# Performance work log

Measured on AMD Instinct MI355X. Metric: run time of the kernel, lower is better.

The kernel has to match this reference:

```python
import jax, jax.numpy as jnp
import numpy as np

T, B = 50, 512
S, A, BEL, H, E, M = 256, 32, 1024, 1024, 1024, 256
MIN_STD = 0.1


def setup_inputs() -> dict:
    key = jax.random.key(0)
    ks = jax.random.split(key, 24)
    def rn(k, shape, scale=1.0):
        return jax.random.normal(k, shape, dtype=jnp.float32) * scale
    w = 0.05  # weight init scale
    return {
        "prev_state": rn(ks[0], (B, S)),
        "actions": rn(ks[1], (T, B, A)),
        "prev_belief": rn(ks[2], (B, BEL)),
        "observations": rn(ks[3], (T, B, E)),
        "nonterminals": jnp.ones((T, B, 1), dtype=jnp.float32),
        "map_embeddings": rn(ks[4], (T, B, M)),
        "map_embeddings_post": rn(ks[5], (T, B, M)),
        "noise_prior": rn(ks[6], (T, B, S)),
        "noise_post": rn(ks[7], (T, B, S)),
        "W_sa": rn(ks[8], (BEL, S + A + M), w), "b_sa": jnp.zeros((BEL,), jnp.float32),
        "W_ih": rn(ks[9], (3 * BEL, BEL), w), "b_ih": jnp.zeros((3 * BEL,), jnp.float32),
        "W_hh": rn(ks[10], (3 * BEL, BEL), w), "b_hh": jnp.zeros((3 * BEL,), jnp.float32),
        "W_bp": rn(ks[11], (H, BEL), w), "b_bp": jnp.zeros((H,), jnp.float32),
        "W_sp": rn(ks[12], (2 * S, H), w), "b_sp": jnp.zeros((2 * S,), jnp.float32),
        "W_bq": rn(ks[13], (H, BEL + E + M), w), "b_bq": jnp.zeros((H,), jnp.float32),
        "W_sq": rn(ks[14], (2 * S, H), w), "b_sq": jnp.zeros((2 * S,), jnp.float32),
    }


def reference(prev_state, actions, prev_belief, observations, nonterminals,
              map_embeddings, map_embeddings_post, noise_prior, noise_post,
              W_sa, b_sa, W_ih, b_ih, W_hh, b_hh,
              W_bp, b_bp, W_sp, b_sp, W_bq, b_bq, W_sq, b_sq):
    relu = jax.nn.relu
    def lin(x, W, b):
        return x @ W.T + b

    def gru(x, h):  # torch.nn.GRUCell math
        gi = x @ W_ih.T + b_ih
        gh = h @ W_hh.T + b_hh
        i_r, i_z, i_n = jnp.split(gi, 3, axis=1)
        h_r, h_z, h_n = jnp.split(gh, 3, axis=1)
        r = jax.nn.sigmoid(i_r + h_r)
        z = jax.nn.sigmoid(i_z + h_z)
        n = jnp.tanh(i_n + r * h_n)
        return (1.0 - z) * n + z * h

    def std(raw):
        return jnp.minimum(jax.nn.softplus(raw) + MIN_STD, 5.0)

    def step(carry, xs):
        belief, post_state = carry
        a, obs, nt, me, mp, np_, nq = xs
        s = post_state * nt
        hid = relu(lin(jnp.concatenate([s, a, me], axis=1), W_sa, b_sa))
        belief = gru(hid, belief)
        # prior p(z_t | h_t)
        hp = relu(lin(belief, W_bp, b_bp))
        p_mean, p_raw = jnp.split(lin(hp, W_sp, b_sp), 2, axis=1)
        p_std = std(p_raw)
        p_state = p_mean + p_std * np_
        # posterior q(z_t | h_t, e_t, m_t)
        hq = relu(lin(jnp.concatenate([belief, obs, mp], axis=1), W_bq, b_bq))
        q_mean, q_raw = jnp.split(lin(hq, W_sq, b_sq), 2, axis=1)
        q_std = std(q_raw)
        q_state = q_mean + q_std * nq
        return (belief, q_state), (belief, p_state, p_mean, p_std, q_state, q_mean, q_std)

    _, outs = jax.lax.scan(
        step, (prev_belief, prev_state),
        (actions, observations, nonterminals, map_embeddings,
         map_embeddings_post, noise_prior, noise_post))
    return outs  # 7 arrays, each (T, B, *)
```

## Files before the change

kernel.cpp:

```cpp
#include <hip/hip_runtime.h>
#include <hip/hip_bf16.h>

#define NT 50
#define NB 512
#define SD 256
#define BD 1024
#define HD 1024
#define ED 1024
#define MD 256
#define NBLK 512
#define GSZ (NBLK * 256)
#define PGSZ (1024 * 256)
#define K1BIG 0x40000000
#define NSLOT 256

typedef __attribute__((ext_vector_type(8))) short bf16x8;
typedef __attribute__((ext_vector_type(4))) float f32x4;

__device__ __forceinline__ void gload_lds16(const void* g, void* l) {
  __builtin_amdgcn_global_load_lds(
      (const __attribute__((address_space(1))) void*)g,
      (__attribute__((address_space(3))) void*)l, 16, 0, 0);
}

__device__ __forceinline__ void cload16_async(const void* a, f32x4* r) {
  asm volatile("global_load_dwordx4 %0, %1, off sc0 sc1" : "=&v"(*r) : "v"(a) : "memory");
}
__device__ __forceinline__ void cload4_async(const void* a, float* r) {
  asm volatile("global_load_dword %0, %1, off sc0 sc1" : "=&v"(*r) : "v"(a) : "memory");
}
#define VMWAIT(N)                                        \
  asm volatile("s_waitcnt vmcnt(" #N ")" ::: "memory");  \
  __builtin_amdgcn_sched_barrier(0);

__device__ __forceinline__ void cstore16(void* g, f32x4 v) {
  asm volatile("global_store_dwordx4 %0, %1, off sc0 sc1" :: "v"(g), "v"(v) : "memory");
}
__device__ __forceinline__ void cstore4(void* g, float v) {
  asm volatile("global_store_dword %0, %1, off sc0 sc1" :: "v"(g), "v"(v) : "memory");
}
__device__ __forceinline__ void cstore2(void* g, unsigned v) {
  asm volatile("global_store_short %0, %1, off sc0 sc1" :: "v"(g), "v"(v) : "memory");
}
__device__ __forceinline__ void ntstore16(void* g, f32x4 v) {
  asm volatile("global_store_dwordx4 %0, %1, off nt" :: "v"(g), "v"(v) : "memory");
}
__device__ __forceinline__ void ntstore4(void* g, float v) {
  asm volatile("global_store_dword %0, %1, off nt" :: "v"(g), "v"(v) : "memory");
}

__device__ __forceinline__ float sigmoidf_(float x) { return 1.0f / (1.0f + __expf(-x)); }
__device__ __forceinline__ float softplusf_(float x) {
  return (x > 0.0f) ? (x + log1pf(__expf(-x))) : log1pf(__expf(x));
}
__device__ __forceinline__ unsigned short bfb(float x) {
  __hip_bfloat16 h = __float2bfloat16(x);
  return __builtin_bit_cast(unsigned short, h);
}

__device__ __forceinline__ void gbar(unsigned* cnt, int slot, int b) {
  asm volatile("s_waitcnt vmcnt(0) lgkmcnt(0)" ::: "memory");
  __syncthreads();
  if (threadIdx.x == 0) {
    unsigned* lc = cnt + slot * 128 + (b & 7) * 16;
    unsigned* gc = cnt + NSLOT * 128 + slot * 16;
    unsigned* fl = cnt + NSLOT * 144 + slot * 16;
    unsigned old = __hip_atomic_fetch_add(lc, 1u, __ATOMIC_RELAXED, __HIP_MEMORY_SCOPE_AGENT);
    if (old == (NBLK / 8 - 1)) {
      unsigned g = __hip_atomic_fetch_add(gc, 1u, __ATOMIC_RELAXED, __HIP_MEMORY_SCOPE_AGENT);
      if (g == 7u)
        __hip_atomic_store(fl, 1u, __ATOMIC_RELAXED, __HIP_MEMORY_SCOPE_AGENT);
    }
    while (__hip_atomic_load(fl, __ATOMIC_RELAXED, __HIP_MEMORY_SCOPE_AGENT) == 0u)
      __builtin_amdgcn_s_sleep(2);
  }
  __syncthreads();
}

__device__ __noinline__ void gemm64(
    int EPI, char* lds,
    const __hip_bfloat16* __restrict__ A1, int lda1,
    const __hip_bfloat16* __restrict__ A2, int lda2, int K1,
    const __hip_bfloat16* __restrict__ Wr, int ldw, int nIter,
    const float* __restrict__ bias, const float* __restrict__ Cadd,
    float* __restrict__ Cf, __hip_bfloat16* __restrict__ Cb, int ldc, int m0) {
  const int tid = threadIdx.x;
  const int lane = tid & 63, w = tid >> 6;
  const int wr = w >> 1, wc = w & 1;
  f32x4 acc[2][2] = {};
  const __hip_bfloat16* a1r = A1 + (size_t)(m0 + lane) * lda1;
  const __hip_bfloat16* a2r = A2 ? (A2 + (size_t)(m0 + lane) * lda2) : a1r;
  const __hip_bfloat16* wrow = Wr + (size_t)lane * ldw;

  f32x4 rA0, rA1;
  auto issueA = [&](int it) {
    const int k0 = it << 6;
    const __hip_bfloat16* as = (k0 < K1) ? (a1r + k0) : (a2r + (k0 - K1));
    cload16_async(as + (2 * w) * 8, &rA0);
    cload16_async(as + (2 * w + 1) * 8, &rA1);
  };
  auto writeA = [&](int it) {
    char* la = lds + ((it & 1) << 14);
    *(f32x4*)(la + (2 * w) * 1024 + lane * 16) = rA0;
    *(f32x4*)(la + (2 * w + 1) * 1024 + lane * 16) = rA1;
  };
  auto stageW = [&](int it) {
    const int k0 = it << 6;
    char* lb = lds + ((it & 1) << 14) + 8192;
    gload_lds16(wrow + k0 + (2 * w) * 8, lb + (2 * w) * 1024);
    gload_lds16(wrow + k0 + (2 * w + 1) * 8, lb + (2 * w + 1) * 1024);
  };

  issueA(0);
  VMWAIT(0)
  writeA(0);
  stageW(0);

  const int kq = lane >> 4, r15 = lane & 15;
  for (int i = 0; i < nIter; ++i) {
    __syncthreads();
    if (i + 1 < nIter) {
      issueA(i + 1);
      stageW(i + 1);
    }
    const char* la = lds + ((i & 1) << 14);
    const char* lb = la + 8192;
#pragma unroll
    for (int s = 0; s < 2; ++s) {
      bf16x8 af[2], bfr[2];
#pragma unroll
      for (int m = 0; m < 2; ++m)
        af[m] = *(const bf16x8*)(la + (size_t)((s * 4 + kq) * 64 + wr * 32 + m * 16 + r15) * 16);
#pragma unroll
      for (int n = 0; n < 2; ++n)
        bfr[n] = *(const bf16x8*)(lb + (size_t)((s * 4 + kq) * 64 + wc * 32 + n * 16 + r15) * 16);
#pragma unroll
      for (int m = 0; m < 2; ++m)
#pragma unroll
        for (int n = 0; n < 2; ++n)
          acc[m][n] = __builtin_amdgcn_mfma_f32_16x16x32_bf16(af[m], bfr[n], acc[m][n], 0, 0, 0);
    }
    if (i + 1 < nIter) {
      VMWAIT(2)
      writeA(i + 1);
    }
  }

  const int rg = lane >> 4;
  float ad[2][2][4];
  if (EPI == 3) {
#pragma unroll
    for (int m = 0; m < 2; ++m)
#pragma unroll
      for (int n = 0; n < 2; ++n) {
        const int col = wc * 32 + n * 16 + r15;
#pragma unroll
        for (int i2 = 0; i2 < 4; ++i2) {
          const int row = m0 + wr * 32 + m * 16 + rg * 4 + i2;
          cload4_async(Cadd + (size_t)row * ldc + col, &ad[m][n][i2]);
        }
      }
    VMWAIT(0)
  }
#pragma unroll
  for (int m = 0; m < 2; ++m) {
#pragma unroll
    for (int n = 0; n < 2; ++n) {
      const int col = wc * 32 + n * 16 + r15;
      const float bv = bias ? bias[col] : 0.0f;
#pragma unroll
      for (int i2 = 0; i2 < 4; ++i2) {
        const int row = m0 + wr * 32 + m * 16 + rg * 4 + i2;
        float v = acc[m][n][i2] + bv;
        if (EPI == 3) v += ad[m][n][i2];
        if (EPI != 0) {
          v = v > 0.0f ? v : 0.0f;
          cstore2(Cb + (size_t)row * ldc + col, (unsigned)bfb(v));
        } else {
          cstore4(Cf + (size_t)row * ldc + col, v);
        }
      }
    }
  }
}

__device__ __noinline__ void gemm_head64(
    char* lds, const __hip_bfloat16* __restrict__ A,
    const __hip_bfloat16* __restrict__ Wr, const float* __restrict__ bias,
    const float* __restrict__ noise, float* __restrict__ st_o, float* __restrict__ mn_o,
    float* __restrict__ sd_o, const float* __restrict__ ntn,
    __hip_bfloat16* __restrict__ sprev, int isq, int n0, int m0) {
  const int tid = threadIdx.x;
  const int lane = tid & 63, w = tid >> 6;
  const int wr = w >> 1, wc = w & 1;
  f32x4 acc[2][2] = {};
  const __hip_bfloat16* ar = A + (size_t)(m0 + lane) * BD;
  const __hip_bfloat16* wrow = Wr + (size_t)lane * BD;

  f32x4 rA0, rA1;
  auto issueA = [&](int it) {
    const int k0 = it << 6;
    cload16_async(ar + k0 + (2 * w) * 8, &rA0);
    cload16_async(ar + k0 + (2 * w + 1) * 8, &rA1);
  };
  auto writeA = [&](int it) {
    char* la = lds + ((it & 1) << 14);
    *(f32x4*)(la + (2 * w) * 1024 + lane * 16) = rA0;
    *(f32x4*)(la + (2 * w + 1) * 1024 + lane * 16) = rA1;
  };
  auto stageW = [&](int it) {
    const int k0 = it << 6;
    char* lb = lds + ((it & 1) << 14) + 8192;
    gload_lds16(wrow + k0 + (2 * w) * 8, lb + (2 * w) * 1024);
    gload_lds16(wrow + k0 + (2 * w + 1) * 8, lb + (2 * w + 1) * 1024);
  };

  issueA(0);
  VMWAIT(0)
  writeA(0);
  stageW(0);

  const int kq = lane >> 4, r15 = lane & 15;
  for (int i = 0; i < 16; ++i) {
    __syncthreads();
    if (i + 1 < 16) {
      issueA(i + 1);
      stageW(i + 1);
    }
    const char* la = lds + ((i & 1) << 14);
    const char* lb = la + 8192;
#pragma unroll
    for (int s = 0; s < 2; ++s) {
      bf16x8 af[2], bfr[2];
#pragma unroll
      for (int m = 0; m < 2; ++m)
        af[m] = *(const bf16x8*)(la + (size_t)((s * 4 + kq) * 64 + wr * 32 + m * 16 + r15) * 16);
#pragma unroll
      for (int n = 0; n < 2; ++n)
        bfr[n] = *(const bf16x8*)(lb + (size_t)((s * 4 + kq) * 64 + wc * 32 + n * 16 + r15) * 16);
#pragma unroll
      for (int m = 0; m < 2; ++m)
#pragma unroll
        for (int n = 0; n < 2; ++n)
          acc[m][n] = __builtin_amdgcn_mfma_f32_16x16x32_bf16(af[m], bfr[n], acc[m][n], 0, 0, 0);
    }
    if (i + 1 < 16) {
      VMWAIT(2)
      writeA(i + 1);
    }
  }

  const int rg = lane >> 4;
  const bool even = (r15 & 1) == 0;
#pragma unroll
  for (int m = 0; m < 2; ++m) {
#pragma unroll
    for (int n = 0; n < 2; ++n) {
      const int col = n0 + wc * 32 + n * 16 + r15;
      const int j = col >> 1;
      const float bv = bias[col];
#pragma unroll
      for (int i2 = 0; i2 < 4; ++i2) {
        const int row = m0 + wr * 32 + m * 16 + rg * 4 + i2;
        float v = acc[m][n][i2] + bv;
        float partner = __shfl_xor(v, 1);
        float mean = even ? v : partner;
        float raw = even ? partner : v;
        float sd = fminf(softplusf_(raw) + 0.1f, 5.0f);
        const size_t o = (size_t)row * SD + j;
        if (even) {
          float st = mean + sd * noise[o];
          ntstore4(mn_o + o, mean);
          ntstore4(st_o + o, st);
          if (isq) cstore2(sprev + o, (unsigned)bfb(st * ntn[row]));
        } else {
          ntstore4(sd_o + o, sd);
        }
      }
    }
  }
}

struct Args {
  const float *prev_state, *actions, *prev_belief, *observations, *nonterminals,
      *me, *mp, *noise_p, *noise_q,
      *W_sa, *b_sa, *W_ih, *b_ih, *W_hh, *b_hh,
      *W_bp, *b_bp, *W_sp, *b_sp, *W_bq, *b_bq, *W_sq, *b_sq;
  float* out;
  unsigned* cnt;
  __hip_bfloat16 *Wsa, *Wih, *Whh, *Wbp, *Wbq, *Wsp, *Wsq;
  __hip_bfloat16 *actme, *obsmp, *sprev, *bel, *hid, *hpb, *hqb;
  float *gi, *gh, *hq_obs;
  float *bsp_ro, *bsq_ro;
};

__global__ __launch_bounds__(256) void prep(Args P) {
  const int gtid = blockIdx.x * 256 + threadIdx.x;
  for (int i = gtid; i < BD * 576; i += PGSZ) {
    int r = i / 576, k = i - r * 576;
    P.Wsa[i] = __float2bfloat16(k < 544 ? P.W_sa[(size_t)r * 544 + k] : 0.0f);
  }
  for (int i = gtid; i < 3 * BD * BD; i += PGSZ) P.Wih[i] = __float2bfloat16(P.W_ih[i]);
  for (int i = gtid; i < 3 * BD * BD; i += PGSZ) P.Whh[i] = __float2bfloat16(P.W_hh[i]);
  for (int i = gtid; i < HD * BD; i += PGSZ) P.Wbp[i] = __float2bfloat16(P.W_bp[i]);
  for (int i = gtid; i < HD * 2304; i += PGSZ) P.Wbq[i] = __float2bfloat16(P.W_bq[i]);
  for (int i = gtid; i < 512 * HD; i += PGSZ) {
    int r = i >> 10, k = i & 1023;
    int dr = (r < 256) ? (2 * r) : (2 * (r - 256) + 1);
    P.Wsp[(size_t)dr * 1024 + k] = __float2bfloat16(P.W_sp[i]);
    P.Wsq[(size_t)dr * 1024 + k] = __float2bfloat16(P.W_sq[i]);
  }
  for (int i = gtid; i < 512; i += PGSZ) {
    int dr = (i < 256) ? (2 * i) : (2 * (i - 256) + 1);
    P.bsp_ro[dr] = P.b_sp[i];
    P.bsq_ro[dr] = P.b_sq[i];
  }
  for (int i = gtid; i < NT * NB * 320; i += PGSZ) {
    int tb = i / 320, j = i - tb * 320;
    float v = (j < 32) ? P.actions[(size_t)tb * 32 + j]
                       : (j < 288 ? P.me[(size_t)tb * 256 + (j - 32)] : 0.0f);
    P.actme[i] = __float2bfloat16(v);
  }
  for (int i = gtid; i < NB * 1280; i += PGSZ) {
    int bb = i / 1280, j = i - bb * 1280;
    float v = (j < ED) ? P.observations[(size_t)bb * ED + j] : P.mp[(size_t)bb * MD + (j - ED)];
    P.obsmp[i] = __float2bfloat16(v);
  }
  for (int i = gtid; i < NB * SD; i += PGSZ) {
    int r = i >> 8;
    P.sprev[i] = __float2bfloat16(P.prev_state[i] * P.nonterminals[r]);
  }
  for (int i = gtid; i < NB * BD; i += PGSZ) P.bel[i] = __float2bfloat16(P.prev_belief[i]);
}

__global__ __launch_bounds__(256, 4) void mega(Args P) {
  __shared__ alignas(16) char lds[32768];
  const int b = blockIdx.x, tid = threadIdx.x;
  const int gtid = b * 256 + tid;

  const size_t o_ps = (size_t)NT * NB * BD;
  const size_t blk = (size_t)NT * NB * SD;

  for (int t = 0; t < NT; ++t) {
    const int s0 = t * 5;
    if (b < 128) {
      const int u = (b & 7) * 16 + (b >> 3), n = u >> 3, m = u & 7;
      gemm64(1, lds, P.sprev, SD, P.actme + (size_t)t * NB * 320, 320, 256,
             P.Wsa + (size_t)n * 64 * 576, 576, 9,
             P.b_sa + n * 64, nullptr, nullptr, P.hid + n * 64, BD, m * 64);
    } else {
      const int b2 = b - 128;
      const int u = (b2 & 7) * 48 + (b2 >> 3), n = u >> 3, m = u & 7;
      gemm64(0, lds, P.bel, BD, nullptr, 0, K1BIG,
             P.Whh + (size_t)n * 64 * BD, BD, 16,
             P.b_hh + n * 64, nullptr, P.gh + n * 64, nullptr, 3 * BD, m * 64);
    }
    gbar(P.cnt, s0 + 0, b);
    if (b < 384) {
      const int u = (b & 7) * 48 + (b >> 3), n = u >> 3, m = u & 7;
      gemm64(0, lds, P.hid, BD, nullptr, 0, K1BIG,
             P.Wih + (size_t)n * 64 * BD, BD, 16,
             P.b_ih + n * 64, nullptr, P.gi + n * 64, nullptr, 3 * BD, m * 64);
    } else if (t == 0) {
      const int b2 = b - 384;
      const int u = (b2 & 7) * 16 + (b2 >> 3), n = u >> 3, m = u & 7;
      gemm64(0, lds, P.obsmp, 1280, nullptr, 0, K1BIG,
             P.Wbq + (size_t)n * 64 * 2304 + 1024, 2304, 20,
             nullptr, nullptr, P.hq_obs + n * 64, nullptr, 1024, m * 64);
    }
    gbar(P.cnt, s0 + 1, b);
    if (gtid < 65536) {
      const int bb = gtid >> 7, j0 = (gtid & 127) << 3;
      const float* gib = P.gi + (size_t)bb * 3072 + j0;
      const float* ghb = P.gh + (size_t)bb * 3072 + j0;
      f32x4 ir0, ir1, iz0, iz1, in0, in1, hr0, hr1, hz0, hz1, hn0, hn1, hbv;
      cload16_async(gib, &ir0);
      cload16_async(gib + 4, &ir1);
      cload16_async(gib + 1024, &iz0);
      cload16_async(gib + 1028, &iz1);
      cload16_async(gib + 2048, &in0);
      cload16_async(gib + 2052, &in1);
      cload16_async(ghb, &hr0);
      cload16_async(ghb + 4, &hr1);
      cload16_async(ghb + 1024, &hz0);
      cload16_async(ghb + 1028, &hz1);
      cload16_async(ghb + 2048, &hn0);
      cload16_async(ghb + 2052, &hn1);
      cload16_async(P.bel + (size_t)bb * BD + j0, &hbv);
      VMWAIT(0)
      bf16x8 hb = __builtin_bit_cast(bf16x8, hbv);
      float o[8];
      unsigned short nb[8];
#pragma unroll
      for (int k = 0; k < 8; ++k) {
        float gr = (k < 4 ? ir0[k] : ir1[k - 4]) + (k < 4 ? hr0[k] : hr1[k - 4]);
        float gz = (k < 4 ? iz0[k] : iz1[k - 4]) + (k < 4 ? hz0[k] : hz1[k - 4]);
        float hn = (k < 4 ? hn0[k] : hn1[k - 4]);
        float in_ = (k < 4 ? in0[k] : in1[k - 4]);
        float r_ = sigmoidf_(gr);
        float z_ = sigmoidf_(gz);
        float n_ = tanhf(in_ + r_ * hn);
        __hip_bfloat16 hv16 = __builtin_bit_cast(__hip_bfloat16, (unsigned short)hb[k]);
        float hv = __bfloat162float(hv16);
        float bel = (1.0f - z_) * n_ + z_ * hv;
        o[k] = bel;
        nb[k] = bfb(bel);
      }
      float* ob = P.out + (size_t)t * NB * BD + (size_t)bb * BD + j0;
      ntstore16(ob, f32x4{o[0], o[1], o[2], o[3]});
      ntstore16(ob + 4, f32x4{o[4], o[5], o[6], o[7]});
      cstore16(P.bel + (size_t)bb * BD + j0, __builtin_bit_cast(f32x4, *(bf16x8*)nb));
    } else if (gtid < 65536 + 40960 && t + 1 < NT) {
      const int k = gtid - 65536;
      const int bb = k / 80, rr = k - bb * 80, j0 = rr << 4;
      const float* src = (j0 < ED)
          ? (P.observations + (size_t)(t + 1) * NB * ED + (size_t)bb * ED + j0)
          : (P.mp + (size_t)(t + 1) * NB * MD + (size_t)bb * MD + (j0 - ED));
      unsigned short nb[16];
#pragma unroll
      for (int q = 0; q < 4; ++q) {
        f32x4 v = *(const f32x4*)(src + q * 4);
#pragma unroll
        for (int kk = 0; kk < 4; ++kk) nb[q * 4 + kk] = bfb(v[kk]);
      }
      cstore16(P.obsmp + (size_t)bb * 1280 + j0, __builtin_bit_cast(f32x4, *(bf16x8*)nb));
      cstore16(P.obsmp + (size_t)bb * 1280 + j0 + 8, __builtin_bit_cast(f32x4, *(bf16x8*)(nb + 8)));
    }
    gbar(P.cnt, s0 + 2, b);
    if (b < 128) {
      const int u = (b & 7) * 16 + (b >> 3), n = u >> 3, m = u & 7;
      gemm64(1, lds, P.bel, BD, nullptr, 0, K1BIG,
             P.Wbp + (size_t)n * 64 * BD, BD, 16,
             P.b_bp + n * 64, nullptr, nullptr, P.hpb + n * 64, HD, m * 64);
    } else if (b < 256) {
      const int b2 = b - 128;
      const int u = (b2 & 7) * 16 + (b2 >> 3), n = u >> 3, m = u & 7;
      gemm64(3, lds, P.bel, BD, nullptr, 0, K1BIG,
             P.Wbq + (size_t)n * 64 * 2304, 2304, 16,
             P.b_bq + n * 64, P.hq_obs + n * 64, nullptr, P.hqb + n * 64, HD, m * 64);
    }
    gbar(P.cnt, s0 + 3, b);
    if (b < 128) {
      const int u = (b & 7) * 16 + (b >> 3);
      const int pq = u >> 6, rr = u & 63, n = rr >> 3, m = rr & 7;
      const float* ntn = P.nonterminals + (size_t)((t + 1 < NT) ? t + 1 : t) * NB;
      const size_t to = (size_t)t * NB * SD;
      if (pq == 0)
        gemm_head64(lds, P.hpb, P.Wsp + (size_t)n * 64 * BD, P.bsp_ro,
                    P.noise_p + to, P.out + o_ps + to, P.out + o_ps + blk + to,
                    P.out + o_ps + 2 * blk + to, ntn, P.sprev, 0, n * 64, m * 64);
      else
        gemm_head64(lds, P.hqb, P.Wsq + (size_t)n * 64 * BD, P.bsq_ro,
                    P.noise_q + to, P.out + o_ps + 3 * blk + to, P.out + o_ps + 4 * blk + to,
                    P.out + o_ps + 5 * blk + to, ntn, P.sprev, 1, n * 64, m * 64);
    } else if (b < 256 && t + 1 < NT) {
      const int b2 = b - 128;
      const int u = (b2 & 7) * 16 + (b2 >> 3), n = u >> 3, m = u & 7;
      gemm64(0, lds, P.obsmp, 1280, nullptr, 0, K1BIG,
             P.Wbq + (size_t)n * 64 * 2304 + 1024, 2304, 20,
             nullptr, nullptr, P.hq_obs + n * 64, nullptr, 1024, m * 64);
    }
    gbar(P.cnt, s0 + 4, b);
  }
}


extern "C" void kernel_launch(void* const* d_in, const int* in_sizes, int n_in,
                              void* d_out, int out_size, void* d_ws, size_t ws_size,
                              hipStream_t stream) {
  Args P;
  P.prev_state = (const float*)d_in[0];
  P.actions = (const float*)d_in[1];
  P.prev_belief = (const float*)d_in[2];
  P.observations = (const float*)d_in[3];
  P.nonterminals = (const float*)d_in[4];
  P.me = (const float*)d_in[5];
  P.mp = (const float*)d_in[6];
  P.noise_p = (const float*)d_in[7];
  P.noise_q = (const float*)d_in[8];
  P.W_sa = (const float*)d_in[9];  P.b_sa = (const float*)d_in[10];
  P.W_ih = (const float*)d_in[11]; P.b_ih = (const float*)d_in[12];
  P.W_hh = (const float*)d_in[13]; P.b_hh = (const float*)d_in[14];
  P.W_bp = (const float*)d_in[15]; P.b_bp = (const float*)d_in[16];
  P.W_sp = (const float*)d_in[17]; P.b_sp = (const float*)d_in[18];
  P.W_bq = (const float*)d_in[19]; P.b_bq = (const float*)d_in[20];
  P.W_sq = (const float*)d_in[21]; P.b_sq = (const float*)d_in[22];
  P.out = (float*)d_out;

  char* p = (char*)d_ws;
  auto carve = [&](size_t bytes) -> char* {
    char* r = p;
    p += (bytes + 255) & ~(size_t)255;
    return r;
  };
  const size_t cnt_bytes = (size_t)NSLOT * 160 * 4;
  P.cnt = (unsigned*)carve(cnt_bytes);
  P.Wsa = (__hip_bfloat16*)carve((size_t)BD * 576 * 2);
  P.Wih = (__hip_bfloat16*)carve((size_t)3 * BD * BD * 2);
  P.Whh = (__hip_bfloat16*)carve((size_t)3 * BD * BD * 2);
  P.Wbp = (__hip_bfloat16*)carve((size_t)HD * BD * 2);
  P.Wbq = (__hip_bfloat16*)carve((size_t)HD * 2304 * 2);
  P.Wsp = (__hip_bfloat16*)carve((size_t)512 * HD * 2);
  P.Wsq = (__hip_bfloat16*)carve((size_t)512 * HD * 2);
  P.bsp_ro = (float*)carve(512 * 4);
  P.bsq_ro = (float*)carve(512 * 4);
  P.actme = (__hip_bfloat16*)carve((size_t)NT * NB * 320 * 2);
  P.obsmp = (__hip_bfloat16*)carve((size_t)NB * 1280 * 2);
  P.sprev = (__hip_bfloat16*)carve((size_t)NB * SD * 2);
  P.bel = (__hip_bfloat16*)carve((size_t)NB * BD * 2);
  P.hid = (__hip_bfloat16*)carve((size_t)NB * BD * 2);
  P.hpb = (__hip_bfloat16*)carve((size_t)NB * HD * 2);
  P.hqb = (__hip_bfloat16*)carve((size_t)NB * HD * 2);
  P.gi = (float*)carve((size_t)NB * 3 * BD * 4);
  P.gh = (float*)carve((size_t)NB * 3 * BD * 4);
  P.hq_obs = (float*)carve((size_t)NB * HD * 4);

  hipMemsetAsync(P.cnt, 0, cnt_bytes, stream);
  prep<<<1024, 256, 0, stream>>>(P);
  mega<<<NBLK, 256, 0, stream>>>(P);
}
```

Measured before the change: 5.713 ms.

## Partition batch rows per XCD and replace grid barriers with per-XCD barriers

Each block reads its hardware XCC id and claims a slot within that XCD. Each XCD then owns 64 batch rows, so each timestep's stages only need a barrier among the blocks of one XCD instead of the whole grid. Because the data a block exchanges now stays inside one XCD's L2, coherent loads and stores drop the sc1 bit and use sc0 only. This relies on the row split matching the XCD mapping and on the startup counting being correct. Each XCD now reads all the weights itself, which adds weight traffic in exchange for lighter synchronisation.

```diff
diff --git a/kernel.cpp b/kernel.cpp
--- a/kernel.cpp
+++ b/kernel.cpp
@@ -9,10 +9,8 @@
 #define ED 1024
 #define MD 256
 #define NBLK 512
-#define GSZ (NBLK * 256)
 #define PGSZ (1024 * 256)
 #define K1BIG 0x40000000
-#define NSLOT 256
 
 typedef __attribute__((ext_vector_type(8))) short bf16x8;
 typedef __attribute__((ext_vector_type(4))) float f32x4;
@@ -23,24 +21,24 @@
       (__attribute__((address_space(3))) void*)l, 16, 0, 0);
 }
 
-__device__ __forceinline__ void cload16_async(const void* a, f32x4* r) {
-  asm volatile("global_load_dwordx4 %0, %1, off sc0 sc1" : "=&v"(*r) : "v"(a) : "memory");
-}
-__device__ __forceinline__ void cload4_async(const void* a, float* r) {
-  asm volatile("global_load_dword %0, %1, off sc0 sc1" : "=&v"(*r) : "v"(a) : "memory");
+__device__ __forceinline__ void aload16(const void* a, f32x4* r) {
+  asm volatile("global_load_dwordx4 %0, %1, off sc0" : "=&v"(*r) : "v"(a) : "memory");
+}
+__device__ __forceinline__ void aload4(const void* a, float* r) {
+  asm volatile("global_load_dword %0, %1, off sc0" : "=&v"(*r) : "v"(a) : "memory");
 }
 #define VMWAIT(N)                                        \
   asm volatile("s_waitcnt vmcnt(" #N ")" ::: "memory");  \
   __builtin_amdgcn_sched_barrier(0);
 
-__device__ __forceinline__ void cstore16(void* g, f32x4 v) {
-  asm volatile("global_store_dwordx4 %0, %1, off sc0 sc1" :: "v"(g), "v"(v) : "memory");
-}
-__device__ __forceinline__ void cstore4(void* g, float v) {
-  asm volatile("global_store_dword %0, %1, off sc0 sc1" :: "v"(g), "v"(v) : "memory");
-}
-__device__ __forceinline__ void cstore2(void* g, unsigned v) {
-  asm volatile("global_store_short %0, %1, off sc0 sc1" :: "v"(g), "v"(v) : "memory");
+__device__ __forceinline__ void astore16(void* g, f32x4 v) {
+  asm volatile("global_store_dwordx4 %0, %1, off sc0" :: "v"(g), "v"(v) : "memory");
+}
+__device__ __forceinline__ void astore4(void* g, float v) {
+  asm volatile("global_store_dword %0, %1, off sc0" :: "v"(g), "v"(v) : "memory");
+}
+__device__ __forceinline__ void astore2(void* g, unsigned v) {
+  asm volatile("global_store_short %0, %1, off sc0" :: "v"(g), "v"(v) : "memory");
 }
 __device__ __forceinline__ void ntstore16(void* g, f32x4 v) {
   asm volatile("global_store_dwordx4 %0, %1, off nt" :: "v"(g), "v"(v) : "memory");
@@ -58,21 +56,14 @@
   return __builtin_bit_cast(unsigned short, h);
 }
 
-__device__ __forceinline__ void gbar(unsigned* cnt, int slot, int b) {
+__device__ __forceinline__ void xbar(unsigned* cnt, int inst, int xcd, int nx) {
   asm volatile("s_waitcnt vmcnt(0) lgkmcnt(0)" ::: "memory");
   __syncthreads();
   if (threadIdx.x == 0) {
-    unsigned* lc = cnt + slot * 128 + (b & 7) * 16;
-    unsigned* gc = cnt + NSLOT * 128 + slot * 16;
-    unsigned* fl = cnt + NSLOT * 144 + slot * 16;
-    unsigned old = __hip_atomic_fetch_add(lc, 1u, __ATOMIC_RELAXED, __HIP_MEMORY_SCOPE_AGENT);
-    if (old == (NBLK / 8 - 1)) {
-      unsigned g = __hip_atomic_fetch_add(gc, 1u, __ATOMIC_RELAXED, __HIP_MEMORY_SCOPE_AGENT);
-      if (g == 7u)
-        __hip_atomic_store(fl, 1u, __ATOMIC_RELAXED, __HIP_MEMORY_SCOPE_AGENT);
-    }
-    while (__hip_atomic_load(fl, __ATOMIC_RELAXED, __HIP_MEMORY_SCOPE_AGENT) == 0u)
-      __builtin_amdgcn_s_sleep(2);
+    unsigned* c = cnt + 256 + (size_t)(inst * 8 + xcd) * 16;
+    __hip_atomic_fetch_add(c, 1u, __ATOMIC_RELAXED, __HIP_MEMORY_SCOPE_AGENT);
+    while (__hip_atomic_load(c, __ATOMIC_RELAXED, __HIP_MEMORY_SCOPE_AGENT) < (unsigned)nx)
+      __builtin_amdgcn_s_sleep(4);
   }
   __syncthreads();
 }
@@ -96,8 +87,8 @@
   auto issueA = [&](int it) {
     const int k0 = it << 6;
     const __hip_bfloat16* as = (k0 < K1) ? (a1r + k0) : (a2r + (k0 - K1));
-    cload16_async(as + (2 * w) * 8, &rA0);
-    cload16_async(as + (2 * w + 1) * 8, &rA1);
+    aload16(as + (2 * w) * 8, &rA0);
+    aload16(as + (2 * w + 1) * 8, &rA1);
   };
   auto writeA = [&](int it) {
     char* la = lds + ((it & 1) << 14);
@@ -111,6 +102,7 @@
     gload_lds16(wrow + k0 + (2 * w + 1) * 8, lb + (2 * w + 1) * 1024);
   };
 
+  __syncthreads();
   issueA(0);
   VMWAIT(0)
   writeA(0);
@@ -157,7 +149,7 @@
 #pragma unroll
         for (int i2 = 0; i2 < 4; ++i2) {
           const int row = m0 + wr * 32 + m * 16 + rg * 4 + i2;
-          cload4_async(Cadd + (size_t)row * ldc + col, &ad[m][n][i2]);
+          aload4(Cadd + (size_t)row * ldc + col, &ad[m][n][i2]);
         }
       }
     VMWAIT(0)
@@ -175,9 +167,9 @@
         if (EPI == 3) v += ad[m][n][i2];
         if (EPI != 0) {
           v = v > 0.0f ? v : 0.0f;
-          cstore2(Cb + (size_t)row * ldc + col, (unsigned)bfb(v));
+          astore2(Cb + (size_t)row * ldc + col, (unsigned)bfb(v));
         } else {
-          cstore4(Cf + (size_t)row * ldc + col, v);
+          astore4(Cf + (size_t)row * ldc + col, v);
         }
       }
     }
@@ -200,8 +192,8 @@
   f32x4 rA0, rA1;
   auto issueA = [&](int it) {
     const int k0 = it << 6;
-    cload16_async(ar + k0 + (2 * w) * 8, &rA0);
-    cload16_async(ar + k0 + (2 * w + 1) * 8, &rA1);
+    aload16(ar + k0 + (2 * w) * 8, &rA0);
+    aload16(ar + k0 + (2 * w + 1) * 8, &rA1);
   };
   auto writeA = [&](int it) {
     char* la = lds + ((it & 1) << 14);
@@ -215,6 +207,7 @@
     gload_lds16(wrow + k0 + (2 * w + 1) * 8, lb + (2 * w + 1) * 1024);
   };
 
+  __syncthreads();
   issueA(0);
   VMWAIT(0)
   writeA(0);
@@ -272,7 +265,7 @@
           float st = mean + sd * noise[o];
           ntstore4(mn_o + o, mean);
           ntstore4(st_o + o, st);
-          if (isq) cstore2(sprev + o, (unsigned)bfb(st * ntn[row]));
+          if (isq) astore2(sprev + o, (unsigned)bfb(st * ntn[row]));
         } else {
           ntstore4(sd_o + o, sd);
         }
@@ -335,58 +328,83 @@
 
 __global__ __launch_bounds__(256, 4) void mega(Args P) {
   __shared__ alignas(16) char lds[32768];
-  const int b = blockIdx.x, tid = threadIdx.x;
-  const int gtid = b * 256 + tid;
-
+  __shared__ int sh[3];
+  const int tid = threadIdx.x;
+
+  if (tid == 0) {
+    unsigned x;
+    asm volatile("s_getreg_b32 %0, hwreg(HW_REG_XCC_ID)" : "=s"(x));
+    x &= 7u;
+    unsigned s = __hip_atomic_fetch_add(P.cnt + x * 16, 1u, __ATOMIC_RELAXED,
+                                        __HIP_MEMORY_SCOPE_AGENT);
+    sh[0] = (int)x;
+    sh[1] = (int)s;
+  }
+  __syncthreads();
+  const int xcd = sh[0], slot = sh[1];
+
+  if (tid == 0) {
+    __hip_atomic_fetch_add(P.cnt + 128, 1u, __ATOMIC_RELAXED, __HIP_MEMORY_SCOPE_AGENT);
+    while (__hip_atomic_load(P.cnt + 128, __ATOMIC_RELAXED, __HIP_MEMORY_SCOPE_AGENT) <
+           (unsigned)NBLK)
+      __builtin_amdgcn_s_sleep(4);
+    sh[2] = (int)__hip_atomic_load(P.cnt + xcd * 16, __ATOMIC_RELAXED,
+                                   __HIP_MEMORY_SCOPE_AGENT);
+  }
+  __syncthreads();
+  const int nx = sh[2];
+  const int m0 = xcd * 64;
   const size_t o_ps = (size_t)NT * NB * BD;
   const size_t blk = (size_t)NT * NB * SD;
 
   for (int t = 0; t < NT; ++t) {
-    const int s0 = t * 5;
-    if (b < 128) {
-      const int u = (b & 7) * 16 + (b >> 3), n = u >> 3, m = u & 7;
-      gemm64(1, lds, P.sprev, SD, P.actme + (size_t)t * NB * 320, 320, 256,
-             P.Wsa + (size_t)n * 64 * 576, 576, 9,
-             P.b_sa + n * 64, nullptr, nullptr, P.hid + n * 64, BD, m * 64);
-    } else {
-      const int b2 = b - 128;
-      const int u = (b2 & 7) * 48 + (b2 >> 3), n = u >> 3, m = u & 7;
-      gemm64(0, lds, P.bel, BD, nullptr, 0, K1BIG,
-             P.Whh + (size_t)n * 64 * BD, BD, 16,
-             P.b_hh + n * 64, nullptr, P.gh + n * 64, nullptr, 3 * BD, m * 64);
-    }
-    gbar(P.cnt, s0 + 0, b);
-    if (b < 384) {
-      const int u = (b & 7) * 48 + (b >> 3), n = u >> 3, m = u & 7;
-      gemm64(0, lds, P.hid, BD, nullptr, 0, K1BIG,
-             P.Wih + (size_t)n * 64 * BD, BD, 16,
-             P.b_ih + n * 64, nullptr, P.gi + n * 64, nullptr, 3 * BD, m * 64);
-    } else if (t == 0) {
-      const int b2 = b - 384;
-      const int u = (b2 & 7) * 16 + (b2 >> 3), n = u >> 3, m = u & 7;
-      gemm64(0, lds, P.obsmp, 1280, nullptr, 0, K1BIG,
-             P.Wbq + (size_t)n * 64 * 2304 + 1024, 2304, 20,
-             nullptr, nullptr, P.hq_obs + n * 64, nullptr, 1024, m * 64);
-    }
-    gbar(P.cnt, s0 + 1, b);
-    if (gtid < 65536) {
-      const int bb = gtid >> 7, j0 = (gtid & 127) << 3;
-      const float* gib = P.gi + (size_t)bb * 3072 + j0;
-      const float* ghb = P.gh + (size_t)bb * 3072 + j0;
+    const int inst = t * 5;
+    for (int tt = slot; tt < 64; tt += nx) {
+      if (tt < 16) {
+        const int n = tt;
+        gemm64(1, lds, P.sprev, SD, P.actme + (size_t)t * NB * 320, 320, 256,
+               P.Wsa + (size_t)n * 64 * 576, 576, 9,
+               P.b_sa + n * 64, nullptr, nullptr, P.hid + n * 64, BD, m0);
+      } else {
+        const int n = tt - 16;
+        gemm64(0, lds, P.bel, BD, nullptr, 0, K1BIG,
+               P.Whh + (size_t)n * 64 * BD, BD, 16,
+               P.b_hh + n * 64, nullptr, P.gh + n * 64, nullptr, 3 * BD, m0);
+      }
+    }
+    xbar(P.cnt, inst + 0, xcd, nx);
+    for (int tt = slot; tt < 64; tt += nx) {
+      if (tt < 48) {
+        const int n = tt;
+        gemm64(0, lds, P.hid, BD, nullptr, 0, K1BIG,
+               P.Wih + (size_t)n * 64 * BD, BD, 16,
+               P.b_ih + n * 64, nullptr, P.gi + n * 64, nullptr, 3 * BD, m0);
+      } else {
+        const int n = tt - 48;
+        gemm64(0, lds, P.obsmp, 1280, nullptr, 0, K1BIG,
+               P.Wbq + (size_t)n * 64 * 2304 + 1024, 2304, 20,
+               nullptr, nullptr, P.hq_obs + n * 64, nullptr, 1024, m0);
+      }
+    }
+    xbar(P.cnt, inst + 1, xcd, nx);
+    for (int u = slot * 256 + tid; u < 8192; u += nx * 256) {
+      const int r = m0 + (u >> 7), j0 = (u & 127) << 3;
+      const float* gib = P.gi + (size_t)r * 3072 + j0;
+      const float* ghb = P.gh + (size_t)r * 3072 + j0;
       f32x4 ir0, ir1, iz0, iz1, in0, in1, hr0, hr1, hz0, hz1, hn0, hn1, hbv;
-      cload16_async(gib, &ir0);
-      cload16_async(gib + 4, &ir1);
-      cload16_async(gib + 1024, &iz0);
-      cload16_async(gib + 1028, &iz1);
-      cload16_async(gib + 2048, &in0);
-      cload16_async(gib + 2052, &in1);
-      cload16_async(ghb, &hr0);
-      cload16_async(ghb + 4, &hr1);
-      cload16_async(ghb + 1024, &hz0);
-      cload16_async(ghb + 1028, &hz1);
-      cload16_async(ghb + 2048, &hn0);
-      cload16_async(ghb + 2052, &hn1);
-      cload16_async(P.bel + (size_t)bb * BD + j0, &hbv);
+      aload16(gib, &ir0);
+      aload16(gib + 4, &ir1);
+      aload16(gib + 1024, &iz0);
+      aload16(gib + 1028, &iz1);
+      aload16(gib + 2048, &in0);
+      aload16(gib + 2052, &in1);
+      aload16(ghb, &hr0);
+      aload16(ghb + 4, &hr1);
+      aload16(ghb + 1024, &hz0);
+      aload16(ghb + 1028, &hz1);
+      aload16(ghb + 2048, &hn0);
+      aload16(ghb + 2052, &hn1);
+      aload16(P.bel + (size_t)r * BD + j0, &hbv);
       VMWAIT(0)
       bf16x8 hb = __builtin_bit_cast(bf16x8, hbv);
       float o[8];
@@ -406,61 +424,60 @@
         o[k] = bel;
         nb[k] = bfb(bel);
       }
-      float* ob = P.out + (size_t)t * NB * BD + (size_t)bb * BD + j0;
+      float* ob = P.out + (size_t)t * NB * BD + (size_t)r * BD + j0;
       ntstore16(ob, f32x4{o[0], o[1], o[2], o[3]});
       ntstore16(ob + 4, f32x4{o[4], o[5], o[6], o[7]});
-      cstore16(P.bel + (size_t)bb * BD + j0, __builtin_bit_cast(f32x4, *(bf16x8*)nb));
-    } else if (gtid < 65536 + 40960 && t + 1 < NT) {
-      const int k = gtid - 65536;
-      const int bb = k / 80, rr = k - bb * 80, j0 = rr << 4;
-      const float* src = (j0 < ED)
-          ? (P.observations + (size_t)(t + 1) * NB * ED + (size_t)bb * ED + j0)
-          : (P.mp + (size_t)(t + 1) * NB * MD + (size_t)bb * MD + (j0 - ED));
-      unsigned short nb[16];
-#pragma unroll
-      for (int q = 0; q < 4; ++q) {
-        f32x4 v = *(const f32x4*)(src + q * 4);
-#pragma unroll
-        for (int kk = 0; kk < 4; ++kk) nb[q * 4 + kk] = bfb(v[kk]);
-      }
-      cstore16(P.obsmp + (size_t)bb * 1280 + j0, __builtin_bit_cast(f32x4, *(bf16x8*)nb));
-      cstore16(P.obsmp + (size_t)bb * 1280 + j0 + 8, __builtin_bit_cast(f32x4, *(bf16x8*)(nb + 8)));
-    }
-    gbar(P.cnt, s0 + 2, b);
-    if (b < 128) {
-      const int u = (b & 7) * 16 + (b >> 3), n = u >> 3, m = u & 7;
-      gemm64(1, lds, P.bel, BD, nullptr, 0, K1BIG,
-             P.Wbp + (size_t)n * 64 * BD, BD, 16,
-             P.b_bp + n * 64, nullptr, nullptr, P.hpb + n * 64, HD, m * 64);
-    } else if (b < 256) {
-      const int b2 = b - 128;
-      const int u = (b2 & 7) * 16 + (b2 >> 3), n = u >> 3, m = u & 7;
-      gemm64(3, lds, P.bel, BD, nullptr, 0, K1BIG,
-             P.Wbq + (size_t)n * 64 * 2304, 2304, 16,
-             P.b_bq + n * 64, P.hq_obs + n * 64, nullptr, P.hqb + n * 64, HD, m * 64);
-    }
-    gbar(P.cnt, s0 + 3, b);
-    if (b < 128) {
-      const int u = (b & 7) * 16 + (b >> 3);
-      const int pq = u >> 6, rr = u & 63, n = rr >> 3, m = rr & 7;
+      astore16(P.bel + (size_t)r * BD + j0, __builtin_bit_cast(f32x4, *(bf16x8*)nb));
+    }
+    if (t + 1 < NT) {
+      for (int v = slot * 256 + tid; v < 5120; v += nx * 256) {
+        const int r = m0 + v / 80, c0 = (v % 80) << 4;
+        const float* src = (c0 < ED)
+            ? (P.observations + (size_t)(t + 1) * NB * ED + (size_t)r * ED + c0)
+            : (P.mp + (size_t)(t + 1) * NB * MD + (size_t)r * MD + (c0 - ED));
+        unsigned short nb[16];
+#pragma unroll
+        for (int q = 0; q < 4; ++q) {
+          f32x4 vv = *(const f32x4*)(src + q * 4);
+#pragma unroll
+          for (int kk = 0; kk < 4; ++kk) nb[q * 4 + kk] = bfb(vv[kk]);
+        }
+        astore16(P.obsmp + (size_t)r * 1280 + c0, __builtin_bit_cast(f32x4, *(bf16x8*)nb));
+        astore16(P.obsmp + (size_t)r * 1280 + c0 + 8,
+                 __builtin_bit_cast(f32x4, *(bf16x8*)(nb + 8)));
+      }
+    }
+    xbar(P.cnt, inst + 2, xcd, nx);
+    for (int tt = slot; tt < 32; tt += nx) {
+      if (tt < 16) {
+        const int n = tt;
+        gemm64(1, lds, P.bel, BD, nullptr, 0, K1BIG,
+               P.Wbp + (size_t)n * 64 * BD, BD, 16,
+               P.b_bp + n * 64, nullptr, nullptr, P.hpb + n * 64, HD, m0);
+      } else {
+        const int n = tt - 16;
+        gemm64(3, lds, P.bel, BD, nullptr, 0, K1BIG,
+               P.Wbq + (size_t)n * 64 * 2304, 2304, 16,
+               P.b_bq + n * 64, P.hq_obs + n * 64, nullptr, P.hqb + n * 64, HD, m0);
+      }
+    }
+    xbar(P.cnt, inst + 3, xcd, nx);
+    {
       const float* ntn = P.nonterminals + (size_t)((t + 1 < NT) ? t + 1 : t) * NB;
       const size_t to = (size_t)t * NB * SD;
-      if (pq == 0)
-        gemm_head64(lds, P.hpb, P.Wsp + (size_t)n * 64 * BD, P.bsp_ro,
-                    P.noise_p + to, P.out + o_ps + to, P.out + o_ps + blk + to,
-                    P.out + o_ps + 2 * blk + to, ntn, P.sprev, 0, n * 64, m * 64);
-      else
-        gemm_head64(lds, P.hqb, P.Wsq + (size_t)n * 64 * BD, P.bsq_ro,
-                    P.noise_q + to, P.out + o_ps + 3 * blk + to, P.out + o_ps + 4 * blk + to,
-                    P.out + o_ps + 5 * blk + to, ntn, P.sprev, 1, n * 64, m * 64);
-    } else if (b < 256 && t + 1 < NT) {
-      const int b2 = b - 128;
-      const int u = (b2 & 7) * 16 + (b2 >> 3), n = u >> 3, m = u & 7;
-      gemm64(0, lds, P.obsmp, 1280, nullptr, 0, K1BIG,
-             P.Wbq + (size_t)n * 64 * 2304 + 1024, 2304, 20,
-             nullptr, nullptr, P.hq_obs + n * 64, nullptr, 1024, m * 64);
-    }
-    gbar(P.cnt, s0 + 4, b);
+      for (int tt = slot; tt < 16; tt += nx) {
+        if (tt < 8)
+          gemm_head64(lds, P.hpb, P.Wsp + (size_t)tt * 64 * BD, P.bsp_ro,
+                      P.noise_p + to, P.out + o_ps + to, P.out + o_ps + blk + to,
+                      P.out + o_ps + 2 * blk + to, ntn, P.sprev, 0, tt * 64, m0);
+        else
+          gemm_head64(lds, P.hqb, P.Wsq + (size_t)(tt - 8) * 64 * BD, P.bsq_ro,
+                      P.noise_q + to, P.out + o_ps + 3 * blk + to,
+                      P.out + o_ps + 4 * blk + to, P.out + o_ps + 5 * blk + to,
+                      ntn, P.sprev, 1, (tt - 8) * 64, m0);
+      }
+    }
+    xbar(P.cnt, inst + 4, xcd, nx);
   }
 }
 
@@ -493,7 +510,7 @@
     p += (bytes + 255) & ~(size_t)255;
     return r;
   };
-  const size_t cnt_bytes = (size_t)NSLOT * 160 * 4;
+  const size_t cnt_bytes = (size_t)65536 * 4;
   P.cnt = (unsigned*)carve(cnt_bytes);
   P.Wsa = (__hip_bfloat16*)carve((size_t)BD * 576 * 2);
   P.Wih = (__hip_bfloat16*)carve((size_t)3 * BD * BD * 2);
```

Result: faster. 5.488 ms (-3.9%).
